# Kernel tuning notes

Hardware: AMD Instinct MI355X
Metric: run time of the kernel (lower is better)

The kernel has to match this reference:

```python
import jax, jax.numpy as jnp
import numpy as np

N_NODES = 50000


def gcn_conv(x, W, b, row, col, num_nodes):
    """PyG-style GCNConv: out = D^{-1/2}(A+I)D^{-1/2} (x @ W) + b.

    row/col already include self-loops. x: [N, Fin], W: [Fin, Fout].
    """
    h = x @ W  # [N, Fout]
    deg = jax.ops.segment_sum(jnp.ones_like(col, dtype=h.dtype), col,
                              num_segments=num_nodes)  # in-degree incl. self-loop
    dinv = jnp.where(deg > 0, jax.lax.rsqrt(deg), 0.0)
    norm = dinv[row] * dinv[col]  # [E]
    msgs = h[row] * norm[:, None]  # gather + scale, [E, Fout]
    out = jax.ops.segment_sum(msgs, col, num_segments=num_nodes)  # scatter-add
    return out + b


def setup_inputs() -> dict:
    key = jax.random.key(0)
    k1, k2, k3, k4 = jax.random.split(key, 4)
    Fin, Fh, Fout = 128, 128, 64
    E = 800000
    x = jax.random.normal(k1, (N_NODES, Fin), dtype=jnp.float32)
    edge_index = jax.random.randint(k2, (2, E), 0, N_NODES, dtype=jnp.int64)
    # Glorot-ish init for weights
    W1 = jax.random.normal(k3, (Fin, Fh), dtype=jnp.float32) / np.sqrt(Fin)
    b1 = jnp.zeros((Fh,), dtype=jnp.float32)
    W2 = jax.random.normal(k4, (Fh, Fout), dtype=jnp.float32) / np.sqrt(Fh)
    b2 = jnp.zeros((Fout,), dtype=jnp.float32)
    return {"x": x, "edge_index": edge_index, "W1": W1, "b1": b1,
            "W2": W2, "b2": b2}


def reference(x, edge_index, W1, b1, W2, b2):
    n = x.shape[0]
    # add self-loops once (shared by both conv layers)
    loops = jnp.arange(n, dtype=edge_index.dtype)
    row = jnp.concatenate([edge_index[0], loops])
    col = jnp.concatenate([edge_index[1], loops])
    h = jax.nn.relu(gcn_conv(x, W1, b1, row, col, n))
    # dropout(p=0.5) is identity in eval mode (self.training == False)
    return gcn_conv(h, W2, b2, row, col, n)
```

## Files before the change

### kernel.cpp

```cpp
#include <hip/hip_runtime.h>


constexpr int KD = 128;
constexpr int CHUNK = 2048;
constexpr int BCAP = 6144;

using short8  = __attribute__((ext_vector_type(8))) short;
using float4v = __attribute__((ext_vector_type(4))) float;


__device__ __forceinline__ unsigned short f2bf(float f) {
    unsigned int u = __float_as_uint(f);
    u = (u + 0x7fffu + ((u >> 16) & 1u)) >> 16;
    return (unsigned short)u;
}

__device__ __forceinline__ float2 bfpair(unsigned int u) {
    float2 f;
    f.x = __uint_as_float(u << 16);
    f.y = __uint_as_float(u & 0xffff0000u);
    return f;
}

__device__ __forceinline__ unsigned int packbf(float x, float y) {
    return (unsigned int)f2bf(x) | ((unsigned int)f2bf(y) << 16);
}

__device__ __forceinline__ void bfsplit(float x, unsigned short& h, unsigned short& l) {
    h = f2bf(x);
    float fh = __uint_as_float((unsigned int)h << 16);
    l = f2bf(x - fh);
}

__global__ __launch_bounds__(128) void setup(const float* __restrict__ W1,
                                             unsigned short* __restrict__ Wth1,
                                             unsigned short* __restrict__ Wtl1,
                                             const float* __restrict__ W2,
                                             unsigned short* __restrict__ Wth2,
                                             unsigned short* __restrict__ Wtl2,
                                             int* __restrict__ gcur) {
    int b = blockIdx.x;
    int n = threadIdx.x;
    int k = b & 127;
    if (b == 0) {
        gcur[n] = n * BCAP;
        gcur[n + 128] = (n + 128) * BCAP;
    }
    if (b < 128) {
        float w = W1[k * 128 + n];
        unsigned short h, l;
        bfsplit(w, h, l);
        Wth1[n * KD + k] = h;
        Wtl1[n * KD + k] = l;
    } else if (n < 64) {
        float w = W2[k * 64 + n];
        unsigned short h, l;
        bfsplit(w, h, l);
        Wth2[n * KD + k] = h;
        Wtl2[n * KD + k] = l;
    }
}

__global__ __launch_bounds__(256) void bucket_scatter(const int* __restrict__ row,
                                                      const int* __restrict__ col,
                                                      int* gcur,
                                                      unsigned int* __restrict__ bpack,
                                                      int E) {
    __shared__ int lh[256];
    __shared__ int lbase[256];
    lh[threadIdx.x] = 0;
    __syncthreads();
    int base = blockIdx.x * CHUNK;
#pragma unroll
    for (int r = 0; r < CHUNK / 256; ++r) {
        int e = base + r * 256 + threadIdx.x;
        if (e < E) atomicAdd(&lh[col[e] >> 8], 1);
    }
    __syncthreads();
    int c0 = lh[threadIdx.x];
    lbase[threadIdx.x] = c0 ? atomicAdd(&gcur[threadIdx.x], c0) : 0;
    __syncthreads();
    lh[threadIdx.x] = 0;
    __syncthreads();
#pragma unroll
    for (int r = 0; r < CHUNK / 256; ++r) {
        int e = base + r * 256 + threadIdx.x;
        if (e < E) {
            int c = col[e];
            int b = c >> 8;
            int slot = lbase[b] + atomicAdd(&lh[b], 1);
            bpack[slot] = ((unsigned int)row[e] << 16) | (unsigned int)c;
        }
    }
}

__global__ __launch_bounds__(256) void csr_and_gemm1(
        const unsigned int* __restrict__ bpack, const int* __restrict__ gcur,
        int* __restrict__ rowptr, float* __restrict__ dinv,
        unsigned short* __restrict__ srow, int N, int E, int NBUCKET,
        const float* __restrict__ X,
        const unsigned short* __restrict__ Wth,
        const unsigned short* __restrict__ Wtl,
        unsigned short* __restrict__ G) {
    __shared__ int s[256];
    __shared__ int lh[256];
    __shared__ int lcur[256];
    __shared__ int sh_bstart;

    if ((int)blockIdx.x < NBUCKET) {
        int b = blockIdx.x;
        int t = threadIdx.x;
        int cntb = gcur[t] - t * BCAP;
        s[t] = cntb;
        __syncthreads();
        for (int off = 1; off < 256; off <<= 1) {
            int tv = (t >= off) ? s[t - off] : 0;
            __syncthreads();
            s[t] += tv;
            __syncthreads();
        }
        if (t == b) sh_bstart = s[t] - cntb;
        if (b == 0 && t == 0) rowptr[N] = E;
        lh[t] = 0;
        __syncthreads();
        int bstart = sh_bstart;
        int nE = gcur[b] - b * BCAP;
        int base = b * BCAP;
        for (int i = t; i < nE; i += 256)
            atomicAdd(&lh[bpack[base + i] & 255], 1);
        __syncthreads();
        int v = lh[t];
        s[t] = v;
        __syncthreads();
        for (int off = 1; off < 256; off <<= 1) {
            int tv = (t >= off) ? s[t - off] : 0;
            __syncthreads();
            s[t] += tv;
            __syncthreads();
        }
        int myStart = bstart + s[t] - v;
        int node = (b << 8) + t;
        if (node < N) {
            rowptr[node] = myStart;
            dinv[node] = rsqrtf(1.0f + (float)v);
        }
        lcur[t] = myStart;
        __syncthreads();
        for (int i = t; i < nE; i += 256) {
            unsigned int p = bpack[base + i];
            int slot = atomicAdd(&lcur[p & 255], 1);
            srow[slot] = (unsigned short)(p >> 16);
        }
    } else {
        constexpr int FOUT = 128, NT = 8;
        int wave = threadIdx.x >> 6;
        int lane = threadIdx.x & 63;
        int row0 = (((int)blockIdx.x - NBUCKET) * 4 + wave) * 16;
        if (row0 >= N) return;
        int m = lane & 15;
        int quad = lane >> 4;

        float4v acc[NT];
#pragma unroll
        for (int ct = 0; ct < NT; ++ct) acc[ct] = (float4v){0.f, 0.f, 0.f, 0.f};

        const float* xrow = X + (size_t)(row0 + m) * KD + quad * 8;

#pragma unroll
        for (int ks = 0; ks < 4; ++ks) {
            float4 xa = *(const float4*)(xrow + ks * 32);
            float4 xb = *(const float4*)(xrow + ks * 32 + 4);
            float xs[8] = {xa.x, xa.y, xa.z, xa.w, xb.x, xb.y, xb.z, xb.w};
            short8 ah, al;
#pragma unroll
            for (int j = 0; j < 8; ++j) {
                unsigned short h, l;
                bfsplit(xs[j], h, l);
                ah[j] = (short)h;
                al[j] = (short)l;
            }
            int koff = ks * 32 + quad * 8;
#pragma unroll
            for (int ct = 0; ct < NT; ++ct) {
                short8 bh = *(const short8*)(Wth + (size_t)(ct * 16 + m) * KD + koff);
                short8 bl = *(const short8*)(Wtl + (size_t)(ct * 16 + m) * KD + koff);
                acc[ct] = __builtin_amdgcn_mfma_f32_16x16x32_bf16(ah, bh, acc[ct], 0, 0, 0);
                acc[ct] = __builtin_amdgcn_mfma_f32_16x16x32_bf16(al, bh, acc[ct], 0, 0, 0);
                acc[ct] = __builtin_amdgcn_mfma_f32_16x16x32_bf16(ah, bl, acc[ct], 0, 0, 0);
            }
        }

#pragma unroll
        for (int r = 0; r < 4; ++r) {
            int row = row0 + quad * 4 + r;
#pragma unroll
            for (int ct = 0; ct < NT; ++ct) {
                G[(size_t)row * FOUT + ct * 16 + m] = f2bf(acc[ct][r]);
            }
        }
    }
}

__global__ __launch_bounds__(256) void gemm_mfma2(const unsigned short* __restrict__ H,
                                                  const unsigned short* __restrict__ Wth,
                                                  const unsigned short* __restrict__ Wtl,
                                                  const float* __restrict__ dinv,
                                                  unsigned short* __restrict__ G, int N) {
    constexpr int FOUT = 64, NT = 4;
    int wave = threadIdx.x >> 6;
    int lane = threadIdx.x & 63;
    int row0 = (blockIdx.x * 4 + wave) * 16;
    if (row0 >= N) return;
    int m = lane & 15;
    int quad = lane >> 4;

    float4v acc[NT];
#pragma unroll
    for (int ct = 0; ct < NT; ++ct) acc[ct] = (float4v){0.f, 0.f, 0.f, 0.f};

    const unsigned short* hrow = H + (size_t)(row0 + m) * KD + quad * 8;

#pragma unroll
    for (int ks = 0; ks < 4; ++ks) {
        short8 a = *(const short8*)(hrow + ks * 32);
        int koff = ks * 32 + quad * 8;
#pragma unroll
        for (int ct = 0; ct < NT; ++ct) {
            short8 bh = *(const short8*)(Wth + (size_t)(ct * 16 + m) * KD + koff);
            short8 bl = *(const short8*)(Wtl + (size_t)(ct * 16 + m) * KD + koff);
            acc[ct] = __builtin_amdgcn_mfma_f32_16x16x32_bf16(a, bh, acc[ct], 0, 0, 0);
            acc[ct] = __builtin_amdgcn_mfma_f32_16x16x32_bf16(a, bl, acc[ct], 0, 0, 0);
        }
    }

#pragma unroll
    for (int r = 0; r < 4; ++r) {
        int row = row0 + quad * 4 + r;
        float s = dinv[row];
#pragma unroll
        for (int ct = 0; ct < 4; ++ct) {
            G[(size_t)row * FOUT + ct * 16 + m] = f2bf(acc[ct][r] * s);
        }
    }
}

template <bool RELU>
__global__ __launch_bounds__(256) void gather128(const int* __restrict__ rowptr,
                                                 const unsigned short* __restrict__ srow,
                                                 const unsigned int* __restrict__ G,
                                                 const float* __restrict__ dinv,
                                                 const float* __restrict__ bias,
                                                 unsigned int* __restrict__ H2,
                                                 int N) {
    int node = (blockIdx.x * 256 + threadIdx.x) >> 6;
    int lane = threadIdx.x & 63;
    if (node >= N) return;
    int beg = rowptr[node];
    int end = rowptr[node + 1];
    float dn = dinv[node];

    float ax, ay;
    {
        float2 s0 = bfpair(G[(size_t)node * 64 + lane]);
        ax = s0.x * dn; ay = s0.y * dn;
    }

    for (int e = beg; e < end; e += 8) {
        unsigned int u[8];
        float dr[8];
#pragma unroll
        for (int j = 0; j < 8; ++j) {
            int idx = e + j;
            idx = (idx < end) ? idx : (end - 1);
            int r = __builtin_amdgcn_readfirstlane((int)srow[idx]);
            dr[j] = dinv[r];
            const unsigned int* p = G + (size_t)r * 64;
            u[j] = p[lane];
        }
        float sx = 0.f, sy = 0.f;
#pragma unroll
        for (int j = 0; j < 8; ++j) {
            unsigned int uv = (e + j < end) ? u[j] : 0u;
            float2 v = bfpair(uv);
            sx = fmaf(dr[j], v.x, sx);
            sy = fmaf(dr[j], v.y, sy);
        }
        ax += sx; ay += sy;
    }
    float2 bv = ((const float2*)bias)[lane];
    float ox = ax * dn + bv.x;
    float oy = ay * dn + bv.y;
    if (RELU) { ox = fmaxf(ox, 0.f); oy = fmaxf(oy, 0.f); }
    __builtin_nontemporal_store(packbf(ox, oy), &H2[(size_t)node * 64 + lane]);
}

template <bool RELU>
__global__ __launch_bounds__(256) void gather64(const int* __restrict__ rowptr,
                                                const unsigned short* __restrict__ srow,
                                                const unsigned int* __restrict__ G,
                                                const float* __restrict__ dinv,
                                                const float* __restrict__ bias,
                                                float* __restrict__ O, int N) {
    int tid = blockIdx.x * 256 + threadIdx.x;
    int node = tid >> 5;
    int lane = threadIdx.x & 31;
    if (node >= N) return;
    int beg = rowptr[node];
    int end = rowptr[node + 1];

    float2 s0 = bfpair(G[(size_t)node * 32 + lane]);
    float ax = s0.x, ay = s0.y;

    for (int e = beg; e < end; e += 8) {
        unsigned int u[8];
#pragma unroll
        for (int j = 0; j < 8; ++j) {
            int idx = e + j;
            idx = (idx < end) ? idx : (end - 1);
            int r = (int)srow[idx];
            u[j] = G[(size_t)r * 32 + lane];
        }
        float sx = 0.f, sy = 0.f;
#pragma unroll
        for (int j = 0; j < 8; ++j) {
            unsigned int uv = (e + j < end) ? u[j] : 0u;
            float2 v = bfpair(uv);
            sx += v.x; sy += v.y;
        }
        ax += sx; ay += sy;
    }
    float s = dinv[node];
    float2 bv = ((const float2*)bias)[lane];
    float ox = ax * s + bv.x;
    float oy = ay * s + bv.y;
    if (RELU) { ox = fmaxf(ox, 0.f); oy = fmaxf(oy, 0.f); }
    float2 o = make_float2(ox, oy);
    unsigned long long p;
    __builtin_memcpy(&p, &o, 8);
    __builtin_nontemporal_store(p, (unsigned long long*)&((float2*)O)[(size_t)node * 32 + lane]);
}

extern "C" void kernel_launch(void* const* d_in, const int* in_sizes, int n_in,
                              void* d_out, int out_size, void* d_ws, size_t ws_size,
                              hipStream_t stream) {
    const float* x  = (const float*)d_in[0];
    const int*   ei = (const int*)d_in[1];
    const float* W1 = (const float*)d_in[2];
    const float* b1 = (const float*)d_in[3];
    const float* W2 = (const float*)d_in[4];
    const float* b2 = (const float*)d_in[5];
    float* out = (float*)d_out;

    int N = in_sizes[0] / 128;
    int E = in_sizes[1] / 2;
    const int* row = ei;
    const int* col = ei + E;

    char* ws = (char*)d_ws;
    float* dinv   = (float*)(ws + 0x000000);
    int*   rowptr = (int*)  (ws + 0x080000);
    int*   gcur   = (int*)  (ws + 0x0F9000);
    unsigned short* srow = (unsigned short*)(ws + 0x100000);
    unsigned short* g1 = (unsigned short*)(ws + 0x440000);
    unsigned short* wth1 = (unsigned short*)(ws + 0x10C0000);
    unsigned short* wtl1 = (unsigned short*)(ws + 0x10D0000);
    unsigned short* wth2 = (unsigned short*)(ws + 0x10E0000);
    unsigned short* wtl2 = (unsigned short*)(ws + 0x10F0000);
    unsigned short* h2 = (unsigned short*)(ws + 0x1200000);
    unsigned short* g2 = (unsigned short*)(ws + 0x2C00000);
    unsigned int* bpack = (unsigned int*)(ws + 0x1200000);

    int NB_BKT  = (E + CHUNK - 1) / CHUNK;
    int NBUCKET = (N + 255) / 256;
    int NB_GEMM1 = (N + 63) / 64;

    setup<<<256, 128, 0, stream>>>(W1, wth1, wtl1, W2, wth2, wtl2, gcur);
    bucket_scatter<<<NB_BKT, 256, 0, stream>>>(row, col, gcur, bpack, E);
    csr_and_gemm1<<<NBUCKET + NB_GEMM1, 256, 0, stream>>>(
        bpack, gcur, rowptr, dinv, srow, N, E, NBUCKET, x, wth1, wtl1, g1);

    int nb;
    nb = (N + 3) / 4;
    gather128<true><<<nb, 256, 0, stream>>>(rowptr, srow, (const unsigned int*)g1,
                                            dinv, b1, (unsigned int*)h2, N);

    nb = (N + 63) / 64;
    gemm_mfma2<<<nb, 256, 0, stream>>>(h2, wth2, wtl2, dinv, g2, N);
    nb = (N + 7) / 8;
    gather64<false><<<nb, 256, 0, stream>>>(rowptr, srow, (const unsigned int*)g2,
                                            dinv, b2, out, N);
}
```

Measured before the change: 197.5 us.

## Pack two nodes per wave in gathers and fuse weight setup into scatter

The weight bf16 split kernel is merged into the bucket scatter launch as extra blocks, and the bucket cursors become zero-based counters cleared by a memset, which removes one kernel launch. Both gather kernels now handle two (or four) nodes per 64-lane wave with wider 8-byte loads per lane. Edge indices and dinv values are loaded cooperatively once per wave and broadcast with shuffles, where before each lane reloaded the same index. The aim is higher memory-level parallelism and fewer scalar index loads, at the cost of divergence when nodes sharing a wave have different degrees.

After: 194.3 us. About the same (-1.6%).

```diff
diff --git a/kernel.cpp b/kernel.cpp
--- a/kernel.cpp
+++ b/kernel.cpp
@@ -32,45 +32,37 @@
     l = f2bf(x - fh);
 }
 
-__global__ __launch_bounds__(128) void setup(const float* __restrict__ W1,
-                                             unsigned short* __restrict__ Wth1,
-                                             unsigned short* __restrict__ Wtl1,
-                                             const float* __restrict__ W2,
-                                             unsigned short* __restrict__ Wth2,
-                                             unsigned short* __restrict__ Wtl2,
-                                             int* __restrict__ gcur) {
-    int b = blockIdx.x;
-    int n = threadIdx.x;
-    int k = b & 127;
-    if (b == 0) {
-        gcur[n] = n * BCAP;
-        gcur[n + 128] = (n + 128) * BCAP;
-    }
-    if (b < 128) {
-        float w = W1[k * 128 + n];
-        unsigned short h, l;
-        bfsplit(w, h, l);
-        Wth1[n * KD + k] = h;
-        Wtl1[n * KD + k] = l;
-    } else if (n < 64) {
-        float w = W2[k * 64 + n];
-        unsigned short h, l;
-        bfsplit(w, h, l);
-        Wth2[n * KD + k] = h;
-        Wtl2[n * KD + k] = l;
-    }
-}
-
-__global__ __launch_bounds__(256) void bucket_scatter(const int* __restrict__ row,
-                                                      const int* __restrict__ col,
-                                                      int* gcur,
-                                                      unsigned int* __restrict__ bpack,
-                                                      int E) {
+__global__ __launch_bounds__(256) void scatter_setup(
+        const int* __restrict__ row, const int* __restrict__ col,
+        int* gcur, unsigned int* __restrict__ bpack, int E, int NBS,
+        const float* __restrict__ W1, unsigned short* __restrict__ Wth1,
+        unsigned short* __restrict__ Wtl1,
+        const float* __restrict__ W2, unsigned short* __restrict__ Wth2,
+        unsigned short* __restrict__ Wtl2) {
     __shared__ int lh[256];
     __shared__ int lbase[256];
+
+    if ((int)blockIdx.x >= NBS) {
+        int id = ((int)blockIdx.x - NBS) * 256 + threadIdx.x;
+        unsigned short h, l;
+        if (id < 16384) {
+            int k = id >> 7, n = id & 127;
+            bfsplit(W1[id], h, l);
+            Wth1[n * KD + k] = h;
+            Wtl1[n * KD + k] = l;
+        } else {
+            int id2 = id - 16384;
+            int k = id2 >> 6, n = id2 & 63;
+            bfsplit(W2[id2], h, l);
+            Wth2[n * KD + k] = h;
+            Wtl2[n * KD + k] = l;
+        }
+        return;
+    }
+
     lh[threadIdx.x] = 0;
     __syncthreads();
-    int base = blockIdx.x * CHUNK;
+    int base = (int)blockIdx.x * CHUNK;
 #pragma unroll
     for (int r = 0; r < CHUNK / 256; ++r) {
         int e = base + r * 256 + threadIdx.x;
@@ -78,7 +70,7 @@
     }
     __syncthreads();
     int c0 = lh[threadIdx.x];
-    lbase[threadIdx.x] = c0 ? atomicAdd(&gcur[threadIdx.x], c0) : 0;
+    lbase[threadIdx.x] = c0 ? (threadIdx.x * BCAP + atomicAdd(&gcur[threadIdx.x], c0)) : 0;
     __syncthreads();
     lh[threadIdx.x] = 0;
     __syncthreads();
@@ -110,7 +102,7 @@
     if ((int)blockIdx.x < NBUCKET) {
         int b = blockIdx.x;
         int t = threadIdx.x;
-        int cntb = gcur[t] - t * BCAP;
+        int cntb = gcur[t];
         s[t] = cntb;
         __syncthreads();
         for (int off = 1; off < 256; off <<= 1) {
@@ -124,7 +116,7 @@
         lh[t] = 0;
         __syncthreads();
         int bstart = sh_bstart;
-        int nE = gcur[b] - b * BCAP;
+        int nE = gcur[b];
         int base = b * BCAP;
         for (int i = t; i < nE; i += 256)
             atomicAdd(&lh[bpack[base + i] & 255], 1);
@@ -251,47 +243,70 @@
                                                  const float* __restrict__ dinv,
                                                  const float* __restrict__ bias,
                                                  unsigned int* __restrict__ H2,
-                                                 int N) {
-    int node = (blockIdx.x * 256 + threadIdx.x) >> 6;
+                                                 int N, int E) {
+    int tid = blockIdx.x * 256 + (int)threadIdx.x;
+    int node = tid >> 5;
     int lane = threadIdx.x & 63;
-    if (node >= N) return;
-    int beg = rowptr[node];
-    int end = rowptr[node + 1];
-    float dn = dinv[node];
-
-    float ax, ay;
-    {
-        float2 s0 = bfpair(G[(size_t)node * 64 + lane]);
-        ax = s0.x * dn; ay = s0.y * dn;
-    }
-
-    for (int e = beg; e < end; e += 8) {
-        unsigned int u[8];
-        float dr[8];
-#pragma unroll
-        for (int j = 0; j < 8; ++j) {
-            int idx = e + j;
-            idx = (idx < end) ? idx : (end - 1);
-            int r = __builtin_amdgcn_readfirstlane((int)srow[idx]);
-            dr[j] = dinv[r];
-            const unsigned int* p = G + (size_t)r * 64;
-            u[j] = p[lane];
-        }
-        float sx = 0.f, sy = 0.f;
-#pragma unroll
-        for (int j = 0; j < 8; ++j) {
-            unsigned int uv = (e + j < end) ? u[j] : 0u;
-            float2 v = bfpair(uv);
-            sx = fmaf(dr[j], v.x, sx);
-            sy = fmaf(dr[j], v.y, sy);
-        }
-        ax += sx; ay += sy;
-    }
-    float2 bv = ((const float2*)bias)[lane];
+    int l32 = lane & 31;
+    bool valid = node < N;
+    int nc = valid ? node : (N - 1);
+    int beg = rowptr[nc];
+    int end = rowptr[nc + 1];
+    int deg = valid ? (end - beg) : 0;
+    float dn = dinv[nc];
+
+    uint2 s0 = ((const uint2*)G)[(size_t)nc * 32 + l32];
+    float2 p0 = bfpair(s0.x), p1 = bfpair(s0.y);
+    float ax = p0.x * dn, ay = p0.y * dn, az = p1.x * dn, aw = p1.y * dn;
+
+    int degmax = max(deg, __shfl_xor(deg, 32));
+
+    for (int w = 0; w < degmax; w += 32) {
+        int li = w + l32;
+        li = (li < deg) ? li : (deg > 0 ? deg - 1 : 0);
+        li += beg;
+        li = (li < E) ? li : (E - 1);
+        int rv = (int)srow[li];
+        float dv = dinv[rv];
+        int lim = degmax - w;
+        for (int g = 0; g < 32 && g < lim; g += 8) {
+            uint2 u[8];
+            float dr[8];
+#pragma unroll
+            for (int j = 0; j < 8; ++j) {
+                int src = (lane & 32) | (g + j);
+                int r = __shfl(rv, src);
+                dr[j] = __shfl(dv, src);
+                u[j] = ((const uint2*)G)[(size_t)r * 32 + l32];
+            }
+            float sx = 0.f, sy = 0.f, sz = 0.f, sw = 0.f;
+#pragma unroll
+            for (int j = 0; j < 8; ++j) {
+                bool ok = (w + g + j) < deg;
+                unsigned int ux = ok ? u[j].x : 0u;
+                unsigned int uy = ok ? u[j].y : 0u;
+                float2 v0 = bfpair(ux), v1 = bfpair(uy);
+                sx = fmaf(dr[j], v0.x, sx);
+                sy = fmaf(dr[j], v0.y, sy);
+                sz = fmaf(dr[j], v1.x, sz);
+                sw = fmaf(dr[j], v1.y, sw);
+            }
+            ax += sx; ay += sy; az += sz; aw += sw;
+        }
+    }
+    if (!valid) return;
+    float4 bv = ((const float4*)bias)[l32];
     float ox = ax * dn + bv.x;
     float oy = ay * dn + bv.y;
-    if (RELU) { ox = fmaxf(ox, 0.f); oy = fmaxf(oy, 0.f); }
-    __builtin_nontemporal_store(packbf(ox, oy), &H2[(size_t)node * 64 + lane]);
+    float oz = az * dn + bv.z;
+    float ow = aw * dn + bv.w;
+    if (RELU) {
+        ox = fmaxf(ox, 0.f); oy = fmaxf(oy, 0.f);
+        oz = fmaxf(oz, 0.f); ow = fmaxf(ow, 0.f);
+    }
+    unsigned long long pv =
+        ((unsigned long long)packbf(oz, ow) << 32) | (unsigned long long)packbf(ox, oy);
+    __builtin_nontemporal_store(pv, (unsigned long long*)H2 + (size_t)nc * 32 + l32);
 }
 
 template <bool RELU>
@@ -300,44 +315,64 @@
                                                 const unsigned int* __restrict__ G,
                                                 const float* __restrict__ dinv,
                                                 const float* __restrict__ bias,
-                                                float* __restrict__ O, int N) {
-    int tid = blockIdx.x * 256 + threadIdx.x;
-    int node = tid >> 5;
-    int lane = threadIdx.x & 31;
-    if (node >= N) return;
-    int beg = rowptr[node];
-    int end = rowptr[node + 1];
-
-    float2 s0 = bfpair(G[(size_t)node * 32 + lane]);
-    float ax = s0.x, ay = s0.y;
-
-    for (int e = beg; e < end; e += 8) {
-        unsigned int u[8];
-#pragma unroll
-        for (int j = 0; j < 8; ++j) {
-            int idx = e + j;
-            idx = (idx < end) ? idx : (end - 1);
-            int r = (int)srow[idx];
-            u[j] = G[(size_t)r * 32 + lane];
-        }
-        float sx = 0.f, sy = 0.f;
-#pragma unroll
-        for (int j = 0; j < 8; ++j) {
-            unsigned int uv = (e + j < end) ? u[j] : 0u;
-            float2 v = bfpair(uv);
-            sx += v.x; sy += v.y;
-        }
-        ax += sx; ay += sy;
-    }
-    float s = dinv[node];
-    float2 bv = ((const float2*)bias)[lane];
+                                                float* __restrict__ O, int N, int E) {
+    int tid = blockIdx.x * 256 + (int)threadIdx.x;
+    int node = tid >> 4;
+    int lane = threadIdx.x & 63;
+    int l16 = lane & 15;
+    bool valid = node < N;
+    int nc = valid ? node : (N - 1);
+    int beg = rowptr[nc];
+    int end = rowptr[nc + 1];
+    int deg = valid ? (end - beg) : 0;
+
+    uint2 s0 = ((const uint2*)G)[(size_t)nc * 16 + l16];
+    float2 p0 = bfpair(s0.x), p1 = bfpair(s0.y);
+    float ax = p0.x, ay = p0.y, az = p1.x, aw = p1.y;
+
+    int dm = max(deg, __shfl_xor(deg, 16));
+    dm = max(dm, __shfl_xor(dm, 32));
+
+    for (int w = 0; w < dm; w += 16) {
+        int li = w + l16;
+        li = (li < deg) ? li : (deg > 0 ? deg - 1 : 0);
+        li += beg;
+        li = (li < E) ? li : (E - 1);
+        int rv = (int)srow[li];
+        int lim = dm - w;
+        for (int g = 0; g < 16 && g < lim; g += 8) {
+            uint2 u[8];
+#pragma unroll
+            for (int j = 0; j < 8; ++j) {
+                int src = (lane & 48) | (g + j);
+                int r = __shfl(rv, src);
+                u[j] = ((const uint2*)G)[(size_t)r * 16 + l16];
+            }
+            float sx = 0.f, sy = 0.f, sz = 0.f, sw = 0.f;
+#pragma unroll
+            for (int j = 0; j < 8; ++j) {
+                bool ok = (w + g + j) < deg;
+                unsigned int ux = ok ? u[j].x : 0u;
+                unsigned int uy = ok ? u[j].y : 0u;
+                float2 v0 = bfpair(ux), v1 = bfpair(uy);
+                sx += v0.x; sy += v0.y; sz += v1.x; sw += v1.y;
+            }
+            ax += sx; ay += sy; az += sz; aw += sw;
+        }
+    }
+    if (!valid) return;
+    float s = dinv[nc];
+    float4 bv = ((const float4*)bias)[l16];
     float ox = ax * s + bv.x;
     float oy = ay * s + bv.y;
-    if (RELU) { ox = fmaxf(ox, 0.f); oy = fmaxf(oy, 0.f); }
-    float2 o = make_float2(ox, oy);
-    unsigned long long p;
-    __builtin_memcpy(&p, &o, 8);
-    __builtin_nontemporal_store(p, (unsigned long long*)&((float2*)O)[(size_t)node * 32 + lane]);
+    float oz = az * s + bv.z;
+    float ow = aw * s + bv.w;
+    if (RELU) {
+        ox = fmaxf(ox, 0.f); oy = fmaxf(oy, 0.f);
+        oz = fmaxf(oz, 0.f); ow = fmaxf(ow, 0.f);
+    }
+    float4v o = {ox, oy, oz, ow};
+    __builtin_nontemporal_store(o, (float4v*)O + (size_t)nc * 16 + l16);
 }
 
 extern "C" void kernel_launch(void* const* d_in, const int* in_sizes, int n_in,
@@ -373,20 +408,22 @@
     int NB_BKT  = (E + CHUNK - 1) / CHUNK;
     int NBUCKET = (N + 255) / 256;
     int NB_GEMM1 = (N + 63) / 64;
-
-    setup<<<256, 128, 0, stream>>>(W1, wth1, wtl1, W2, wth2, wtl2, gcur);
-    bucket_scatter<<<NB_BKT, 256, 0, stream>>>(row, col, gcur, bpack, E);
+    int NB_SETUP = 96;
+
+    hipMemsetAsync(gcur, 0, 256 * sizeof(int), stream);
+    scatter_setup<<<NB_BKT + NB_SETUP, 256, 0, stream>>>(
+        row, col, gcur, bpack, E, NB_BKT, W1, wth1, wtl1, W2, wth2, wtl2);
     csr_and_gemm1<<<NBUCKET + NB_GEMM1, 256, 0, stream>>>(
         bpack, gcur, rowptr, dinv, srow, N, E, NBUCKET, x, wth1, wtl1, g1);
 
     int nb;
-    nb = (N + 3) / 4;
+    nb = (N + 7) / 8;
     gather128<true><<<nb, 256, 0, stream>>>(rowptr, srow, (const unsigned int*)g1,
-                                            dinv, b1, (unsigned int*)h2, N);
+                                            dinv, b1, (unsigned int*)h2, N, E);
 
     nb = (N + 63) / 64;
     gemm_mfma2<<<nb, 256, 0, stream>>>(h2, wth2, wtl2, dinv, g2, N);
-    nb = (N + 7) / 8;
+    nb = (N + 15) / 16;
     gather64<false><<<nb, 256, 0, stream>>>(rowptr, srow, (const unsigned int*)g2,
-                                            dinv, b2, out, N);
-}
+                                            dinv, b2, out, N, E);
+}
```
